# Kernel optimization log

Hardware: AMD Instinct MI355X
Metric: run time of the kernel (lower is better)

The kernel has to match this reference:

```python
import jax, jax.numpy as jnp
import numpy as np

N, E, F_IN, F_OUT = 50000, 800000, 256, 64


def setup_inputs() -> dict:
    key = jax.random.key(0)
    k1, k2, k3, k4 = jax.random.split(key, 4)
    x = jax.random.normal(k1, (N, F_IN), dtype=jnp.float32)
    adj = jax.random.randint(k2, (2, E), 0, N, dtype=jnp.int32)
    # GCNConv parameters (glorot-ish init)
    W = jax.random.normal(k3, (F_IN, F_OUT), dtype=jnp.float32) / np.sqrt(F_IN)
    b = jnp.zeros((F_OUT,), dtype=jnp.float32)
    return {"x": x, "adj": adj, "W": W, "b": b}


def reference(x, adj, W, b):
    n = x.shape[0]
    # PyG GCNConv: add self-loops, symmetric normalization D^-1/2 A D^-1/2
    loop = jnp.arange(n, dtype=adj.dtype)
    src = jnp.concatenate([adj[0], loop])  # [E+N]
    dst = jnp.concatenate([adj[1], loop])  # [E+N]
    deg = jax.ops.segment_sum(jnp.ones_like(dst, dtype=x.dtype), dst, num_segments=n)
    dinv = jax.lax.rsqrt(deg)  # deg >= 1 due to self-loops
    norm = dinv[src] * dinv[dst]  # [E+N]
    h = x @ W  # [N, F_OUT] — transform before propagate (GCNConv order)
    msg = h[src] * norm[:, None]  # [E+N, F_OUT]
    out = jax.ops.segment_sum(msg, dst, num_segments=n) + b
    return jax.nn.relu(out)
```

## Files before the change

kernel.cpp:

```cpp
#include <hip/hip_runtime.h>

#define F_IN 256
#define F_OUT 64
#define BSH 7
#define BINW 128
#define NBINS_CAP 512
#define BATCH 4096
#define CSTRIDE 16
#define MAXBIN_CAP 2560

typedef __attribute__((ext_vector_type(8))) short short8;
typedef __attribute__((ext_vector_type(4))) float f32x4;

__device__ inline float bf_lo(unsigned u) { return __uint_as_float(u << 16); }
__device__ inline float bf_hi(unsigned u) { return __uint_as_float(u & 0xFFFF0000u); }
__device__ inline unsigned cvt_pk_bf16(float lo, float hi) {
    unsigned r;
    asm("v_cvt_pk_bf16_f32 %0, %1, %2" : "=v"(r) : "v"(lo), "v"(hi));
    return r;
}
__device__ inline short8 pack_cvt(float4 a, float4 b) {
    union { unsigned u[4]; short8 s; } r;
    r.u[0] = cvt_pk_bf16(a.x, a.y);
    r.u[1] = cvt_pk_bf16(a.z, a.w);
    r.u[2] = cvt_pk_bf16(b.x, b.y);
    r.u[3] = cvt_pk_bf16(b.z, b.w);
    return r.s;
}

__global__ __launch_bounds__(256) void bin_count(const int* __restrict__ adj,
                                                 unsigned* __restrict__ staging,
                                                 int* __restrict__ cursor,
                                                 int E, int nbins, int maxBin) {
    __shared__ int cnt[NBINS_CAP];
    __shared__ int base[NBINS_CAP];
    const int tid = threadIdx.x;
    for (int i = tid; i < NBINS_CAP; i += 256) cnt[i] = 0;
    __syncthreads();

    const int e0 = blockIdx.x * BATCH + tid * 16;
    int S[16], D[16], sl[16];
    int nv = 0;
    if (e0 + 16 <= E) {
#pragma unroll
        for (int k = 0; k < 4; k++) {
            *(int4*)&S[k * 4] = *(const int4*)&adj[e0 + k * 4];
            *(int4*)&D[k * 4] = *(const int4*)&adj[E + e0 + k * 4];
        }
        nv = 16;
    } else if (e0 < E) {
        for (int k = 0; k < 16 && e0 + k < E; k++) {
            S[k] = adj[e0 + k];
            D[k] = adj[E + e0 + k];
            nv++;
        }
    }
#pragma unroll
    for (int j = 0; j < 16; j++) {
        if (j < nv) sl[j] = atomicAdd(&cnt[D[j] >> BSH], 1);
    }
    __syncthreads();
    for (int i = tid; i < nbins; i += 256) {
        int cv = cnt[i];
        base[i] = cv ? atomicAdd(&cursor[i * CSTRIDE], cv) : 0;
    }
    __syncthreads();
#pragma unroll
    for (int j = 0; j < 16; j++) {
        if (j < nv) {
            int b = D[j] >> BSH;
            int pos = base[b] + sl[j];
            if (pos < maxBin)
                staging[(size_t)b * maxBin + pos] =
                    (unsigned)S[j] | ((unsigned)(D[j] & (BINW - 1)) << 16);
        }
    }
}

__global__ __launch_bounds__(512, 4) void gemm_mfma(const float* __restrict__ x,
                                                    const float* __restrict__ W,
                                                    const unsigned* __restrict__ staging,
                                                    const int* __restrict__ cursor,
                                                    unsigned* __restrict__ gu,
                                                    int N, int maxBin) {
    __shared__ unsigned Wf[32 * 64 * 4];
    __shared__ int degL[BINW];
    __shared__ float dinvL[BINW];
    const int b = blockIdx.x;
    const int tid = threadIdx.x;

    if (tid < BINW) degL[tid] = 0;
    for (int p = tid; p < (F_IN / 2) * F_OUT; p += 512) {
        int kp = p >> 6;
        int n = p & 63;
        int k = kp * 2;
        Wf[((k >> 3) * 64 + n) * 4 + ((k & 7) >> 1)] =
            cvt_pk_bf16(W[k * F_OUT + n], W[(k + 1) * F_OUT + n]);
    }
    __syncthreads();

    const int segCnt = min(cursor[b * CSTRIDE], maxBin);
    const unsigned* seg = staging + (size_t)b * maxBin;
    for (int i = tid; i < segCnt; i += 512) atomicAdd(&degL[seg[i] >> 16], 1);
    __syncthreads();
    if (tid < BINW) dinvL[tid] = rsqrtf((float)degL[tid] + 1.0f);
    __syncthreads();

    const int wave = tid >> 6;
    const int lane = tid & 63;
    const int q = lane >> 4;
    const int c = lane & 15;
    const int n0 = b * 128 + wave * 16;
    const int r = min(n0 + c, N - 1);
    const float* p0 = x + (size_t)r * F_IN + q * 8;

    f32x4 acc[4] = {};
#pragma unroll
    for (int s = 0; s < 8; s++) {
        float4 a0 = *(const float4*)(p0 + s * 32);
        float4 a1 = *(const float4*)(p0 + s * 32 + 4);
        short8 ah = pack_cvt(a0, a1);
#pragma unroll
        for (int t = 0; t < 4; t++) {
            short8 bh = *(const short8*)&Wf[((s * 4 + q) * 64 + t * 16 + c) * 4];
            acc[t] = __builtin_amdgcn_mfma_f32_16x16x32_bf16(ah, bh, acc[t], 0, 0, 0);
        }
    }

#pragma unroll
    for (int rr = 0; rr < 4; rr++) {
        int node = n0 + q * 4 + rr;
        float dv = dinvL[wave * 16 + q * 4 + rr];
#pragma unroll
        for (int t = 0; t < 4; t++) {
            float v = acc[t][rr] * dv;
            float o = __shfl_xor(v, 1, 64);
            if (node < N && !(lane & 1)) {
                gu[(size_t)node * 32 + t * 8 + (c >> 1)] = cvt_pk_bf16(v, o);
            }
        }
    }
}

__global__ __launch_bounds__(1024) void gather_bin(const unsigned* __restrict__ staging,
                                                   const int* __restrict__ cursor,
                                                   const unsigned* __restrict__ g32,
                                                   const float* __restrict__ bias,
                                                   float* __restrict__ out,
                                                   int N, int maxBin) {
    __shared__ int cnt[BINW];
    __shared__ int off[BINW];
    __shared__ int wsum[2];
    __shared__ unsigned short binCsr[MAXBIN_CAP];
    const int b = blockIdx.x;
    const int tid = threadIdx.x;
    const int nb0 = b << BSH;

    if (tid < BINW) cnt[tid] = 0;
    __syncthreads();

    const int segCnt = min(cursor[b * CSTRIDE], maxBin);
    const unsigned* seg = staging + (size_t)b * maxBin;

    unsigned ev[3];
    int sl[3];
    int nv = 0;
#pragma unroll
    for (int r = 0; r < 3; r++) {
        int i = tid + r * 1024;
        if (i < segCnt) {
            unsigned e = seg[i];
            ev[r] = e;
            sl[r] = atomicAdd(&cnt[e >> 16], 1);
            nv = r + 1;
        }
    }
    __syncthreads();

    int incl = 0, v = 0;
    if (tid < BINW) {
        v = cnt[tid];
        incl = v;
        const int lane = tid & 63;
        for (int d = 1; d < 64; d <<= 1) {
            int t = __shfl_up(incl, d, 64);
            if (lane >= d) incl += t;
        }
        if (lane == 63) wsum[tid >> 6] = incl;
    }
    __syncthreads();
    if (tid < BINW) off[tid] = incl - v + ((tid >= 64) ? wsum[0] : 0);
    __syncthreads();

#pragma unroll
    for (int r = 0; r < 3; r++) {
        if (r < nv) binCsr[off[ev[r] >> 16] + sl[r]] = (unsigned short)(ev[r] & 0xFFFFu);
    }
    __syncthreads();

    const int wv = tid >> 6;
    const int lane = tid & 63;
    const int grp = lane >> 3;
    const int h = lane & 7;
    const uint4* g4 = (const uint4*)g32;

    for (int t = 0; t < 8; t++) {
        const int node = wv * 8 + t;
        const int gn = nb0 + node;
        if (gn >= N) break;
        const int start = off[node];
        const int deg = cnt[node];

        float a0[8] = {}, a1[8] = {};
        int i = grp;
        for (; i + 8 < deg; i += 16) {
            int s0 = binCsr[start + i], s1 = binCsr[start + i + 8];
            uint4 u0 = g4[(size_t)s0 * 8 + h];
            uint4 u1 = g4[(size_t)s1 * 8 + h];
            a0[0] += bf_lo(u0.x); a0[1] += bf_hi(u0.x);
            a0[2] += bf_lo(u0.y); a0[3] += bf_hi(u0.y);
            a0[4] += bf_lo(u0.z); a0[5] += bf_hi(u0.z);
            a0[6] += bf_lo(u0.w); a0[7] += bf_hi(u0.w);
            a1[0] += bf_lo(u1.x); a1[1] += bf_hi(u1.x);
            a1[2] += bf_lo(u1.y); a1[3] += bf_hi(u1.y);
            a1[4] += bf_lo(u1.z); a1[5] += bf_hi(u1.z);
            a1[6] += bf_lo(u1.w); a1[7] += bf_hi(u1.w);
        }
        if (i < deg) {
            int s0 = binCsr[start + i];
            uint4 u0 = g4[(size_t)s0 * 8 + h];
            a0[0] += bf_lo(u0.x); a0[1] += bf_hi(u0.x);
            a0[2] += bf_lo(u0.y); a0[3] += bf_hi(u0.y);
            a0[4] += bf_lo(u0.z); a0[5] += bf_hi(u0.z);
            a0[6] += bf_lo(u0.w); a0[7] += bf_hi(u0.w);
        }
        float acc[8];
#pragma unroll
        for (int k = 0; k < 8; k++) acc[k] = a0[k] + a1[k];
#pragma unroll
        for (int m = 8; m < 64; m <<= 1) {
#pragma unroll
            for (int k = 0; k < 8; k++) acc[k] += __shfl_xor(acc[k], m, 64);
        }
        if (grp == 0) {
            uint4 us = g4[(size_t)gn * 8 + h];
            float dv = rsqrtf((float)deg + 1.0f);
            float s0 = bf_lo(us.x), s1 = bf_hi(us.x), s2 = bf_lo(us.y), s3 = bf_hi(us.y);
            float s4 = bf_lo(us.z), s5 = bf_hi(us.z), s6 = bf_lo(us.w), s7 = bf_hi(us.w);
            float4 b0 = *(const float4*)&bias[h * 8];
            float4 b1 = *(const float4*)&bias[h * 8 + 4];
            float4 r0, r1;
            r0.x = fmaxf(fmaf(dv, acc[0] + s0, b0.x), 0.0f);
            r0.y = fmaxf(fmaf(dv, acc[1] + s1, b0.y), 0.0f);
            r0.z = fmaxf(fmaf(dv, acc[2] + s2, b0.z), 0.0f);
            r0.w = fmaxf(fmaf(dv, acc[3] + s3, b0.w), 0.0f);
            r1.x = fmaxf(fmaf(dv, acc[4] + s4, b1.x), 0.0f);
            r1.y = fmaxf(fmaf(dv, acc[5] + s5, b1.y), 0.0f);
            r1.z = fmaxf(fmaf(dv, acc[6] + s6, b1.z), 0.0f);
            r1.w = fmaxf(fmaf(dv, acc[7] + s7, b1.w), 0.0f);
            *(float4*)&out[(size_t)gn * F_OUT + h * 8] = r0;
            *(float4*)&out[(size_t)gn * F_OUT + h * 8 + 4] = r1;
        }
    }
}

extern "C" void kernel_launch(void* const* d_in, const int* in_sizes, int n_in,
                              void* d_out, int out_size, void* d_ws, size_t ws_size,
                              hipStream_t stream) {
    const float* x = (const float*)d_in[0];
    const int* adj = (const int*)d_in[1];
    const float* W = (const float*)d_in[2];
    const float* b = (const float*)d_in[3];
    float* out = (float*)d_out;

    const int N = in_sizes[0] / F_IN;
    const int E = in_sizes[1] / 2;
    const int nbins = (N + BINW - 1) >> BSH;
    const int maxBin = MAXBIN_CAP;

    char* ws = (char*)d_ws;
    size_t segCur = (((size_t)nbins * CSTRIDE * 4) + 255) & ~(size_t)255;
    size_t segStg = (((size_t)nbins * maxBin * 4) + 255) & ~(size_t)255;
    int* cursor = (int*)ws;
    unsigned* staging = (unsigned*)(ws + segCur);
    unsigned* g16 = (unsigned*)(ws + segCur + segStg);

    hipMemsetAsync(cursor, 0, segCur, stream);

    bin_count<<<(E + BATCH - 1) / BATCH, 256, 0, stream>>>(adj, staging, cursor,
                                                           E, nbins, maxBin);
    gemm_mfma<<<nbins, 512, 0, stream>>>(x, W, staging, cursor, g16, N, maxBin);
    gather_bin<<<nbins, 1024, 0, stream>>>(staging, cursor, g16, b, out, N, maxBin);
}
```

Before: 143.1 us.

## Assign one node per 8-lane group instead of splitting edges across the wave

Result: faster. 133.0 us (-7.0%).

```diff
diff --git a/kernel.cpp b/kernel.cpp
--- a/kernel.cpp
+++ b/kernel.cpp
@@ -202,21 +202,23 @@
     const int lane = tid & 63;
     const int grp = lane >> 3;
     const int h = lane & 7;
+    const int node = wv * 8 + grp;
+    const int gn = nb0 + node;
     const uint4* g4 = (const uint4*)g32;
 
-    for (int t = 0; t < 8; t++) {
-        const int node = wv * 8 + t;
-        const int gn = nb0 + node;
-        if (gn >= N) break;
+    if (gn < N) {
         const int start = off[node];
         const int deg = cnt[node];
 
         float a0[8] = {}, a1[8] = {};
-        int i = grp;
-        for (; i + 8 < deg; i += 16) {
-            int s0 = binCsr[start + i], s1 = binCsr[start + i + 8];
+        int i = 0;
+        for (; i + 4 <= deg; i += 4) {
+            int s0 = binCsr[start + i], s1 = binCsr[start + i + 1];
+            int s2 = binCsr[start + i + 2], s3 = binCsr[start + i + 3];
             uint4 u0 = g4[(size_t)s0 * 8 + h];
             uint4 u1 = g4[(size_t)s1 * 8 + h];
+            uint4 u2 = g4[(size_t)s2 * 8 + h];
+            uint4 u3 = g4[(size_t)s3 * 8 + h];
             a0[0] += bf_lo(u0.x); a0[1] += bf_hi(u0.x);
             a0[2] += bf_lo(u0.y); a0[3] += bf_hi(u0.y);
             a0[4] += bf_lo(u0.z); a0[5] += bf_hi(u0.z);
@@ -225,8 +227,16 @@
             a1[2] += bf_lo(u1.y); a1[3] += bf_hi(u1.y);
             a1[4] += bf_lo(u1.z); a1[5] += bf_hi(u1.z);
             a1[6] += bf_lo(u1.w); a1[7] += bf_hi(u1.w);
-        }
-        if (i < deg) {
+            a0[0] += bf_lo(u2.x); a0[1] += bf_hi(u2.x);
+            a0[2] += bf_lo(u2.y); a0[3] += bf_hi(u2.y);
+            a0[4] += bf_lo(u2.z); a0[5] += bf_hi(u2.z);
+            a0[6] += bf_lo(u2.w); a0[7] += bf_hi(u2.w);
+            a1[0] += bf_lo(u3.x); a1[1] += bf_hi(u3.x);
+            a1[2] += bf_lo(u3.y); a1[3] += bf_hi(u3.y);
+            a1[4] += bf_lo(u3.z); a1[5] += bf_hi(u3.z);
+            a1[6] += bf_lo(u3.w); a1[7] += bf_hi(u3.w);
+        }
+        for (; i < deg; i++) {
             int s0 = binCsr[start + i];
             uint4 u0 = g4[(size_t)s0 * 8 + h];
             a0[0] += bf_lo(u0.x); a0[1] += bf_hi(u0.x);
@@ -234,33 +244,24 @@
             a0[4] += bf_lo(u0.z); a0[5] += bf_hi(u0.z);
             a0[6] += bf_lo(u0.w); a0[7] += bf_hi(u0.w);
         }
-        float acc[8];
-#pragma unroll
-        for (int k = 0; k < 8; k++) acc[k] = a0[k] + a1[k];
-#pragma unroll
-        for (int m = 8; m < 64; m <<= 1) {
-#pragma unroll
-            for (int k = 0; k < 8; k++) acc[k] += __shfl_xor(acc[k], m, 64);
-        }
-        if (grp == 0) {
-            uint4 us = g4[(size_t)gn * 8 + h];
-            float dv = rsqrtf((float)deg + 1.0f);
-            float s0 = bf_lo(us.x), s1 = bf_hi(us.x), s2 = bf_lo(us.y), s3 = bf_hi(us.y);
-            float s4 = bf_lo(us.z), s5 = bf_hi(us.z), s6 = bf_lo(us.w), s7 = bf_hi(us.w);
-            float4 b0 = *(const float4*)&bias[h * 8];
-            float4 b1 = *(const float4*)&bias[h * 8 + 4];
-            float4 r0, r1;
-            r0.x = fmaxf(fmaf(dv, acc[0] + s0, b0.x), 0.0f);
-            r0.y = fmaxf(fmaf(dv, acc[1] + s1, b0.y), 0.0f);
-            r0.z = fmaxf(fmaf(dv, acc[2] + s2, b0.z), 0.0f);
-            r0.w = fmaxf(fmaf(dv, acc[3] + s3, b0.w), 0.0f);
-            r1.x = fmaxf(fmaf(dv, acc[4] + s4, b1.x), 0.0f);
-            r1.y = fmaxf(fmaf(dv, acc[5] + s5, b1.y), 0.0f);
-            r1.z = fmaxf(fmaf(dv, acc[6] + s6, b1.z), 0.0f);
-            r1.w = fmaxf(fmaf(dv, acc[7] + s7, b1.w), 0.0f);
-            *(float4*)&out[(size_t)gn * F_OUT + h * 8] = r0;
-            *(float4*)&out[(size_t)gn * F_OUT + h * 8 + 4] = r1;
-        }
+
+        uint4 us = g4[(size_t)gn * 8 + h];
+        float dv = rsqrtf((float)deg + 1.0f);
+        float s0 = bf_lo(us.x), s1 = bf_hi(us.x), s2 = bf_lo(us.y), s3 = bf_hi(us.y);
+        float s4 = bf_lo(us.z), s5 = bf_hi(us.z), s6 = bf_lo(us.w), s7 = bf_hi(us.w);
+        float4 b0 = *(const float4*)&bias[h * 8];
+        float4 b1 = *(const float4*)&bias[h * 8 + 4];
+        float4 r0, r1;
+        r0.x = fmaxf(fmaf(dv, a0[0] + a1[0] + s0, b0.x), 0.0f);
+        r0.y = fmaxf(fmaf(dv, a0[1] + a1[1] + s1, b0.y), 0.0f);
+        r0.z = fmaxf(fmaf(dv, a0[2] + a1[2] + s2, b0.z), 0.0f);
+        r0.w = fmaxf(fmaf(dv, a0[3] + a1[3] + s3, b0.w), 0.0f);
+        r1.x = fmaxf(fmaf(dv, a0[4] + a1[4] + s4, b1.x), 0.0f);
+        r1.y = fmaxf(fmaf(dv, a0[5] + a1[5] + s5, b1.y), 0.0f);
+        r1.z = fmaxf(fmaf(dv, a0[6] + a1[6] + s6, b1.z), 0.0f);
+        r1.w = fmaxf(fmaf(dv, a0[7] + a1[7] + s7, b1.w), 0.0f);
+        *(float4*)&out[(size_t)gn * F_OUT + h * 8] = r0;
+        *(float4*)&out[(size_t)gn * F_OUT + h * 8 + 4] = r1;
     }
 }
 
```
